# Optimization experiments

Measured on AMD Instinct MI355X. Metric: run time of the kernel, lower is better.

The kernel has to match this reference:

```python
import jax, jax.numpy as jnp
import numpy as np

MASK_ID = -100
L, D, HID, NH = 10, 768, 3072, 12
DH = D // NH
REACH = 2  # (sliding_window_size - 1) // 2 with window 5


def _layernorm(x, g, b, eps=1e-5):
    mu = x.mean(-1, keepdims=True)
    var = ((x - mu) ** 2).mean(-1, keepdims=True)
    return (x - mu) * jax.lax.rsqrt(var + eps) * g + b


def _adaln(x, temb, w, bb, g, be):
    # AdaLayerNormShiftScale: linear(silu(temb)) -> (scale, shift)
    e = jax.nn.silu(temb) @ w + bb
    scale, shift = jnp.split(e, 2, axis=-1)
    return _layernorm(x, g, be) * (1.0 + scale) + shift


def _timestep_emb(t):
    half = D // 2
    exponent = -np.log(10000.0) * jnp.arange(half, dtype=jnp.float32) / (half - 1.0)
    freq = jnp.exp(exponent)  # [half]
    emb = t.astype(jnp.float32)[..., None] * freq  # [b,s,half]
    return jnp.concatenate([jnp.sin(emb), jnp.cos(emb)], axis=-1)  # [b,s,D]


def setup_inputs():
    key = jax.random.key(0)
    ks = jax.random.split(key, 16)
    b, s = 4, 1024
    # packed token ids: 4 samples of 256 tokens (16x16 grid), last 64 tokens padding
    idx = np.arange(s)
    sid = idx // 256
    hpos = (idx % 256) // 16
    wpos = idx % 16
    sid = np.where(idx >= 960, MASK_ID, sid)
    tok = np.stack([sid, hpos, wpos], axis=-1)  # [s,3]
    token_ids = jnp.asarray(np.broadcast_to(tok, (b, s, 3)).copy(), dtype=jnp.int32)
    t = jax.random.randint(ks[0], (b, 1), 0, L + 1).astype(jnp.int32)
    t = jnp.broadcast_to(t, (b, s))

    def w(k, shape):
        return jax.random.normal(k, shape, jnp.float32) * 0.02

    return dict(
        x=jax.random.normal(ks[1], (b, s, D), jnp.float32),
        t=t,
        token_ids=token_ids,
        proj_in_w=w(ks[2], (D, D)), proj_in_b=jnp.zeros((D,), jnp.float32),
        h_emb=w(ks[3], (64, D)), w_emb=w(ks[4], (64, D)),
        adaln1_w=w(ks[5], (L, D, 2 * D)), adaln1_b=jnp.zeros((L, 2 * D), jnp.float32),
        ln1_g=jnp.ones((L, D), jnp.float32), ln1_b=jnp.zeros((L, D), jnp.float32),
        qkv_w=w(ks[6], (L, D, 3 * D)), qkv_b=jnp.zeros((L, 3 * D), jnp.float32),
        o_w=w(ks[7], (L, D, D)), o_b=jnp.zeros((L, D), jnp.float32),
        adaln2_w=w(ks[8], (L, D, 2 * D)), adaln2_b=jnp.zeros((L, 2 * D), jnp.float32),
        ln2_g=jnp.ones((L, D), jnp.float32), ln2_b=jnp.zeros((L, D), jnp.float32),
        fc1_w=w(ks[9], (L, D, HID)), fc1_b=jnp.zeros((L, HID), jnp.float32),
        fc2_w=w(ks[10], (L, HID, D)), fc2_b=jnp.zeros((L, D), jnp.float32),
        nout_w=w(ks[11], (D, 2 * D)), nout_b=jnp.zeros((2 * D,), jnp.float32),
        nout_g=jnp.ones((D,), jnp.float32), nout_beta=jnp.zeros((D,), jnp.float32),
    )


def _encoder(x, t, token_ids, proj_in_w, proj_in_b, h_emb, w_emb,
             adaln1_w, adaln1_b, ln1_g, ln1_b, qkv_w, qkv_b, o_w, o_b,
             adaln2_w, adaln2_b, ln2_g, ln2_b, fc1_w, fc1_b, fc2_w, fc2_b,
             nout_w, nout_b, nout_g, nout_beta):
    b, s, _ = x.shape
    sample_ids = token_ids[..., 0]          # [b,s]
    pos = token_ids[..., 1:]                # [b,s,2]
    x = x @ proj_in_w + proj_in_b
    x = x + h_emb[pos[..., 0]] + w_emb[pos[..., 1]]

    # block-sparse mask: same packed sample, Chebyshev sliding window, no padding queries
    same = sample_ids[:, :, None] == sample_ids[:, None, :]              # [b,s,s]
    cheby = jnp.abs(pos[:, :, None, :] - pos[:, None, :, :]).max(-1)      # [b,s,s]
    notpad_q = (sample_ids != MASK_ID)[:, :, None]
    mask = same & (cheby <= REACH) & notpad_q                             # [b,s,s]
    row_valid = mask.any(-1)[..., None]                                   # [b,s,1]

    temb = _timestep_emb(t)  # [b,s,D]
    scale = 1.0 / np.sqrt(DH)
    for i in range(L):
        h1 = _adaln(x, temb, adaln1_w[i], adaln1_b[i], ln1_g[i], ln1_b[i])
        qkv = h1 @ qkv_w[i] + qkv_b[i]
        q, k, v = jnp.split(qkv, 3, axis=-1)
        q = q.reshape(b, s, NH, DH)
        k = k.reshape(b, s, NH, DH)
        v = v.reshape(b, s, NH, DH)
        scores = jnp.einsum('bqhd,bkhd->bhqk', q, k) * scale
        scores = jnp.where(mask[:, None], scores, -1e30)
        attn = jax.nn.softmax(scores, axis=-1)
        o = jnp.einsum('bhqk,bkhd->bqhd', attn, v).reshape(b, s, D)
        o = jnp.where(row_valid, o, 0.0)  # fully-masked (padding) rows -> 0
        x = x + o @ o_w[i] + o_b[i]
        h2 = _adaln(x, temb, adaln2_w[i], adaln2_b[i], ln2_g[i], ln2_b[i])
        x = x + jax.nn.gelu(h2 @ fc1_w[i] + fc1_b[i], approximate=False) @ fc2_w[i] + fc2_b[i]
    x = _adaln(x, temb, nout_w, nout_b, nout_g, nout_beta)
    return x


def reference(x, t, token_ids, proj_in_w, proj_in_b, h_emb, w_emb,
              adaln1_w, adaln1_b, ln1_g, ln1_b, qkv_w, qkv_b, o_w, o_b,
              adaln2_w, adaln2_b, ln2_g, ln2_b, fc1_w, fc1_b, fc2_w, fc2_b,
              nout_w, nout_b, nout_g, nout_beta):
    return _encoder(x, t, token_ids, proj_in_w, proj_in_b, h_emb, w_emb,
                    adaln1_w, adaln1_b, ln1_g, ln1_b, qkv_w, qkv_b, o_w, o_b,
                    adaln2_w, adaln2_b, ln2_g, ln2_b, fc1_w, fc1_b, fc2_w, fc2_b,
                    nout_w, nout_b, nout_g, nout_beta)
```

## Files before the change

### kernel.cpp

```cpp
#include <hip/hip_runtime.h>
#include <hip/hip_bf16.h>
#include <math.h>

#define MASK_ID (-100)
#define SEQ 1024
#define BATCH 4
#define DMODEL 768
#define NHEAD 12
#define DHEAD 64
#define NLAYER 10
#define HIDDEN 3072

typedef unsigned short ushort_t;
typedef unsigned int uint_t;

__device__ __forceinline__ ushort_t f2bf(float f) {
    uint_t u = __float_as_uint(f);
    u = u + 0x7fffu + ((u >> 16) & 1u);
    return (ushort_t)(u >> 16);
}
__device__ __forceinline__ float bf2f(ushort_t u) {
    return __uint_as_float(((uint_t)u) << 16);
}

__device__ __forceinline__ void async_ld16(ushort_t* lds, const ushort_t* g) {
    __builtin_amdgcn_global_load_lds((__attribute__((address_space(1))) const void*)g,
                                     (__attribute__((address_space(3))) void*)lds, 16, 0, 0);
}

#define WAITVM(n) asm volatile("s_waitcnt vmcnt(" #n ")" ::: "memory")

__global__ void temb_silu_kernel(const int* __restrict__ t, float* __restrict__ stemb) {
    int b = blockIdx.x;
    int j = threadIdx.x;
    float tv = (float)t[b * SEQ];
    float freq = expf(-logf(10000.f) * (float)j / 383.f);
    float arg = tv * freq;
    float s = sinf(arg), c = cosf(arg);
    stemb[b * DMODEL + j]       = s / (1.f + expf(-s));
    stemb[b * DMODEL + 384 + j] = c / (1.f + expf(-c));
}

__global__ __launch_bounds__(256)
void adaln_partial_kernel(const float* __restrict__ stemb,
                          const float* __restrict__ a1w,
                          const float* __restrict__ a2w,
                          const float* __restrict__ nw,
                          float* __restrict__ partial) {
    int chunk = blockIdx.x;
    int kc    = blockIdx.y;
    int slot  = blockIdx.z;
    int tid = threadIdx.x;
    int col = chunk * 256 + tid;
    const float* W;
    if (slot == 20) W = nw;
    else {
        int i = slot >> 1;
        W = ((slot & 1) ? a2w : a1w) + (size_t)i * DMODEL * 2 * DMODEL;
    }
    __shared__ float sb[4 * 96];
    for (int idx = tid; idx < 4 * 96; idx += 256) {
        int bb = idx / 96, kk = idx % 96;
        sb[idx] = stemb[bb * DMODEL + kc * 96 + kk];
    }
    __syncthreads();
    const float* Wp = W + (size_t)(kc * 96) * (2 * DMODEL) + col;
    float a0 = 0.f, a1 = 0.f, a2 = 0.f, a3 = 0.f;
    #pragma unroll 4
    for (int kk = 0; kk < 96; ++kk) {
        float w = Wp[(size_t)kk * (2 * DMODEL)];
        a0 = fmaf(sb[kk], w, a0);
        a1 = fmaf(sb[96 + kk], w, a1);
        a2 = fmaf(sb[192 + kk], w, a2);
        a3 = fmaf(sb[288 + kk], w, a3);
    }
    size_t base = ((size_t)(slot * 8 + kc) * 4) * (2 * DMODEL) + col;
    partial[base + 0 * 2 * DMODEL] = a0;
    partial[base + 1 * 2 * DMODEL] = a1;
    partial[base + 2 * 2 * DMODEL] = a2;
    partial[base + 3 * 2 * DMODEL] = a3;
}

__global__ __launch_bounds__(256)
void adaln_reduce_kernel(const float* __restrict__ partial,
                         const float* __restrict__ a1b, const float* __restrict__ a2b,
                         const float* __restrict__ nb,
                         float* __restrict__ e_all) {
    int chunk = blockIdx.x;
    int slot  = blockIdx.y;
    int col = chunk * 256 + threadIdx.x;
    const float* bb;
    if (slot == 20) bb = nb;
    else {
        int i = slot >> 1;
        bb = ((slot & 1) ? a2b : a1b) + i * 2 * DMODEL;
    }
    float bias = bb[col];
    float s0 = bias, s1 = bias, s2 = bias, s3 = bias;
    #pragma unroll
    for (int kc = 0; kc < 8; ++kc) {
        size_t base = ((size_t)(slot * 8 + kc) * 4) * (2 * DMODEL) + col;
        s0 += partial[base + 0 * 2 * DMODEL];
        s1 += partial[base + 1 * 2 * DMODEL];
        s2 += partial[base + 2 * 2 * DMODEL];
        s3 += partial[base + 3 * 2 * DMODEL];
    }
    size_t o = (size_t)slot * 4 * (2 * DMODEL) + col;
    e_all[o + 0 * 2 * DMODEL] = s0;
    e_all[o + 1 * 2 * DMODEL] = s1;
    e_all[o + 2 * 2 * DMODEL] = s2;
    e_all[o + 3 * 2 * DMODEL] = s3;
}

__global__ __launch_bounds__(256)
void transpose_bf16_kernel(const float* __restrict__ in, ushort_t* __restrict__ out,
                           int R, int C) {
    __shared__ float tile[32][33];
    int tx = threadIdx.x & 31, ty = threadIdx.x >> 5;
    int c0 = blockIdx.x * 32, r0 = blockIdx.y * 32;
    #pragma unroll
    for (int i = 0; i < 4; ++i)
        tile[ty + 8 * i][tx] = in[(size_t)(r0 + ty + 8 * i) * C + c0 + tx];
    __syncthreads();
    #pragma unroll
    for (int i = 0; i < 4; ++i)
        out[(size_t)(c0 + ty + 8 * i) * R + r0 + tx] = f2bf(tile[tx][ty + 8 * i]);
}

__global__ __launch_bounds__(256)
void transpose_all_kernel(const float* __restrict__ w0, const float* __restrict__ w1,
                          const float* __restrict__ w2, const float* __restrict__ w3,
                          ushort_t* __restrict__ o0, ushort_t* __restrict__ o1,
                          ushort_t* __restrict__ o2, ushort_t* __restrict__ o3) {
    int layer = blockIdx.y;
    int id = blockIdx.x;
    const float* in; ushort_t* out; int R, C, tile_id, TX;
    if (id < 1728) {
        in = w0 + (size_t)layer * DMODEL * 3 * DMODEL; out = o0 + (size_t)layer * 3 * DMODEL * DMODEL;
        R = DMODEL; C = 3 * DMODEL; tile_id = id; TX = 72;
    } else if (id < 2304) {
        in = w1 + (size_t)layer * DMODEL * DMODEL; out = o1 + (size_t)layer * DMODEL * DMODEL;
        R = DMODEL; C = DMODEL; tile_id = id - 1728; TX = 24;
    } else if (id < 4608) {
        in = w2 + (size_t)layer * DMODEL * HIDDEN; out = o2 + (size_t)layer * HIDDEN * DMODEL;
        R = DMODEL; C = HIDDEN; tile_id = id - 2304; TX = 96;
    } else {
        in = w3 + (size_t)layer * HIDDEN * DMODEL; out = o3 + (size_t)layer * DMODEL * HIDDEN;
        R = HIDDEN; C = DMODEL; tile_id = id - 4608; TX = 24;
    }
    int c0 = (tile_id % TX) * 32, r0 = (tile_id / TX) * 32;
    __shared__ float tile[32][33];
    int tx = threadIdx.x & 31, ty = threadIdx.x >> 5;
    #pragma unroll
    for (int i = 0; i < 4; ++i)
        tile[ty + 8 * i][tx] = in[(size_t)(r0 + ty + 8 * i) * C + c0 + tx];
    __syncthreads();
    #pragma unroll
    for (int i = 0; i < 4; ++i)
        out[(size_t)(c0 + ty + 8 * i) * R + r0 + tx] = f2bf(tile[tx][ty + 8 * i]);
}

__global__ __launch_bounds__(256)
void f32_to_bf16_kernel(const float* __restrict__ in, ushort_t* __restrict__ out, int n8) {
    int i = blockIdx.x * 256 + threadIdx.x;
    if (i >= n8) return;
    float4 a = ((const float4*)in)[2 * i];
    float4 b = ((const float4*)in)[2 * i + 1];
    uint4 o;
    o.x = (uint_t)f2bf(a.x) | ((uint_t)f2bf(a.y) << 16);
    o.y = (uint_t)f2bf(a.z) | ((uint_t)f2bf(a.w) << 16);
    o.z = (uint_t)f2bf(b.x) | ((uint_t)f2bf(b.y) << 16);
    o.w = (uint_t)f2bf(b.z) | ((uint_t)f2bf(b.w) << 16);
    ((uint4*)out)[i] = o;
}

template<int OUT_BF>
__global__ __launch_bounds__(256)
void ln_adaln_kernel(const float* __restrict__ in, void* __restrict__ outv,
                     const float* __restrict__ g, const float* __restrict__ be,
                     const float* __restrict__ e) {
    int row = blockIdx.x;
    int b = row >> 10;
    const float* xr = in + (size_t)row * DMODEL;
    int tid = threadIdx.x;
    float v0 = xr[tid], v1 = xr[tid + 256], v2 = xr[tid + 512];
    float s = v0 + v1 + v2;
    float ss = v0 * v0 + v1 * v1 + v2 * v2;
    #pragma unroll
    for (int o = 32; o; o >>= 1) { s += __shfl_down(s, o); ss += __shfl_down(ss, o); }
    __shared__ float ls[4], lss[4];
    __shared__ float mu_s, rs_s;
    int wid = tid >> 6, lane = tid & 63;
    if (lane == 0) { ls[wid] = s; lss[wid] = ss; }
    __syncthreads();
    if (tid == 0) {
        float S = ls[0] + ls[1] + ls[2] + ls[3];
        float SS = lss[0] + lss[1] + lss[2] + lss[3];
        float mu = S * (1.f / DMODEL);
        float var = SS * (1.f / DMODEL) - mu * mu;
        mu_s = mu;
        rs_s = rsqrtf(var + 1e-5f);
    }
    __syncthreads();
    float mu = mu_s, rs = rs_s;
    const float* esc = e + (size_t)b * (2 * DMODEL);
    #pragma unroll
    for (int j = 0; j < 3; ++j) {
        int c = tid + j * 256;
        float v = (j == 0) ? v0 : (j == 1) ? v1 : v2;
        float y = (v - mu) * rs * g[c] + be[c];
        y = y * (1.f + esc[c]) + esc[DMODEL + c];
        if (OUT_BF) ((ushort_t*)outv)[(size_t)row * DMODEL + c] = f2bf(y);
        else        ((float*)outv)[(size_t)row * DMODEL + c] = y;
    }
}

__device__ __forceinline__ float gelu_exact(float x) {
    return 0.5f * x * (1.f + erff(x * 0.70710678118654752f));
}

template<int BM, int BN, int EPI>
__global__ __launch_bounds__(256, 2)
void gemm_bf16(const ushort_t* __restrict__ A, const ushort_t* __restrict__ Wt,
               const float* __restrict__ bias, void* __restrict__ outv,
               const float* __restrict__ emb_h, const float* __restrict__ emb_w,
               const int* __restrict__ tok,
               int M, int N, int K) {
    constexpr int WM = BM / 2, WN = BN / 2;
    constexpr int FM = WM / 16, FN = WN / 16;
    constexpr int BUF = (BM + BN) * 64;
    constexpr int LPT = (BM + BN) / 32;
    using f32x4  = __attribute__((ext_vector_type(4))) float;
    using bf16x8 = __attribute__((ext_vector_type(8))) short;

    __shared__ __align__(16) ushort_t lds[3 * BUF];

    int tid = threadIdx.x;
    int lane = tid & 63, wid = tid >> 6;
    int wr = wid >> 1, wc = wid & 1;
    int l16 = lane & 15, lg = lane >> 4;
    int sw = l16 & 7;

    int nx = N / BN;
    int cpx = gridDim.x >> 3;
    int wg = blockIdx.x;
    int wgid = (wg & 7) * cpx + (wg >> 3);
    int bx = wgid % nx, by = wgid / nx;
    int bm0 = by * BM, bn0 = bx * BN;

    f32x4 acc[FM][FN];
    #pragma unroll
    for (int m = 0; m < FM; ++m)
        #pragma unroll
        for (int n = 0; n < FN; ++n)
            #pragma unroll
            for (int r = 0; r < 4; ++r) acc[m][n][r] = 0.f;

    const ushort_t* Abase = A + (size_t)bm0 * K;
    const ushort_t* Bbase = Wt + (size_t)bn0 * K;

    #define STAGE(bufi, kt)                                                             \
        do {                                                                            \
            _Pragma("unroll")                                                           \
            for (int s2 = 0; s2 < BM / 32; ++s2) {                                      \
                int ca = s2 * 256 + tid;                                                \
                int rw = ca >> 3, kcs = (ca & 7) ^ (rw & 7);                            \
                async_ld16(&lds[(bufi) * BUF + ca * 8],                                 \
                           Abase + (size_t)rw * K + (kt) * 64 + kcs * 8);               \
            }                                                                           \
            _Pragma("unroll")                                                           \
            for (int s2 = 0; s2 < BN / 32; ++s2) {                                      \
                int ca = s2 * 256 + tid;                                                \
                int rw = ca >> 3, kcs = (ca & 7) ^ (rw & 7);                            \
                async_ld16(&lds[(bufi) * BUF + BM * 64 + ca * 8],                       \
                           Bbase + (size_t)rw * K + (kt) * 64 + kcs * 8);               \
            }                                                                           \
        } while (0)

    int nk = K >> 6;
    STAGE(0, 0);
    STAGE(1, 1);
    int bufi = 0;
    for (int kt = 0; kt < nk; ++kt) {
        int nxt = bufi + 2; if (nxt >= 3) nxt -= 3;
        if (kt + 2 < nk) {
            STAGE(nxt, kt + 2);
            if constexpr (LPT == 4) WAITVM(8); else WAITVM(12);
        } else if (kt + 1 < nk) {
            if constexpr (LPT == 4) WAITVM(4); else WAITVM(6);
        } else {
            WAITVM(0);
        }
        __builtin_amdgcn_s_barrier();
        __builtin_amdgcn_s_setprio(1);
        #pragma unroll
        for (int kk = 0; kk < 2; ++kk) {
            bf16x8 af[FM], bfr[FN];
            #pragma unroll
            for (int m = 0; m < FM; ++m) {
                int row = wr * WM + m * 16 + l16;
                int csw = (kk * 4 + lg) ^ sw;
                af[m] = *(const bf16x8*)&lds[bufi * BUF + row * 64 + csw * 8];
            }
            #pragma unroll
            for (int n = 0; n < FN; ++n) {
                int row = wc * WN + n * 16 + l16;
                int csw = (kk * 4 + lg) ^ sw;
                bfr[n] = *(const bf16x8*)&lds[bufi * BUF + BM * 64 + row * 64 + csw * 8];
            }
            #pragma unroll
            for (int m = 0; m < FM; ++m)
                #pragma unroll
                for (int n = 0; n < FN; ++n)
                    acc[m][n] = __builtin_amdgcn_mfma_f32_16x16x32_bf16(af[m], bfr[n], acc[m][n], 0, 0, 0);
        }
        __builtin_amdgcn_s_setprio(0);
        __builtin_amdgcn_s_barrier();
        ++bufi; if (bufi >= 3) bufi = 0;
    }
    #undef STAGE

    int r0 = bm0 + wr * WM, c0 = bn0 + wc * WN;
    #pragma unroll
    for (int m = 0; m < FM; ++m) {
        #pragma unroll
        for (int n = 0; n < FN; ++n) {
            int cc = c0 + n * 16 + l16;
            float bcol = bias[cc];
            #pragma unroll
            for (int r = 0; r < 4; ++r) {
                int row = r0 + m * 16 + lg * 4 + r;
                float v = acc[m][n][r] + bcol;
                if (EPI == 0) {
                    ((ushort_t*)outv)[(size_t)row * N + cc] = f2bf(v);
                } else if (EPI == 1) {
                    int p0 = tok[row * 3 + 1], p1 = tok[row * 3 + 2];
                    v += emb_h[p0 * DMODEL + cc] + emb_w[p1 * DMODEL + cc];
                    ((float*)outv)[(size_t)row * N + cc] = v;
                } else if (EPI == 2) {
                    float* op = (float*)outv + (size_t)row * N + cc;
                    *op = *op + v;
                } else {
                    ((ushort_t*)outv)[(size_t)row * N + cc] = f2bf(gelu_exact(v));
                }
            }
        }
    }
}

__global__ __launch_bounds__(256)
void attn_kernel(const ushort_t* __restrict__ qkv, const int* __restrict__ tok,
                 ushort_t* __restrict__ o_out) {
    int tid = threadIdx.x;
    int u = tid >> 2, part = tid & 3;
    int q = blockIdx.x * 16 + (u & 15);
    int h = blockIdx.y * 4 + (u >> 4);
    int b = blockIdx.z;
    int m = b * SEQ + q;
    ushort_t* op = o_out + (size_t)m * DMODEL + h * DHEAD + part * 16;
    int sid = tok[m * 3];
    if (sid == MASK_ID) {
        uint4 z = {0u, 0u, 0u, 0u};
        ((uint4*)op)[0] = z;
        ((uint4*)op)[1] = z;
        return;
    }
    int qh = tok[m * 3 + 1], qw = tok[m * 3 + 2];
    const ushort_t* qp = qkv + (size_t)m * (3 * DMODEL) + h * DHEAD + part * 16;
    float qv[16], ov[16];
    {
        uint4 u0 = ((const uint4*)qp)[0];
        uint4 u1 = ((const uint4*)qp)[1];
        qv[0] = bf2f(u0.x & 0xffff); qv[1] = bf2f(u0.x >> 16);
        qv[2] = bf2f(u0.y & 0xffff); qv[3] = bf2f(u0.y >> 16);
        qv[4] = bf2f(u0.z & 0xffff); qv[5] = bf2f(u0.z >> 16);
        qv[6] = bf2f(u0.w & 0xffff); qv[7] = bf2f(u0.w >> 16);
        qv[8]  = bf2f(u1.x & 0xffff); qv[9]  = bf2f(u1.x >> 16);
        qv[10] = bf2f(u1.y & 0xffff); qv[11] = bf2f(u1.y >> 16);
        qv[12] = bf2f(u1.z & 0xffff); qv[13] = bf2f(u1.z >> 16);
        qv[14] = bf2f(u1.w & 0xffff); qv[15] = bf2f(u1.w >> 16);
    }
    #pragma unroll
    for (int i = 0; i < 16; ++i) ov[i] = 0.f;
    float mx = -1e30f, den = 0.f;
    for (int dh = -2; dh <= 2; ++dh) {
        for (int dw = -2; dw <= 2; ++dw) {
            int kq = q + dh * 16 + dw;
            if (kq < 0 || kq >= SEQ) continue;
            int km = b * SEQ + kq;
            if (tok[km * 3] != sid) continue;
            int kh2 = tok[km * 3 + 1], kw2 = tok[km * 3 + 2];
            int adh = kh2 - qh; if (adh < 0) adh = -adh;
            int adw = kw2 - qw; if (adw < 0) adw = -adw;
            if (adh > 2 || adw > 2) continue;
            const ushort_t* kp = qkv + (size_t)km * (3 * DMODEL) + DMODEL + h * DHEAD + part * 16;
            float dot;
            {
                uint4 u0 = ((const uint4*)kp)[0];
                uint4 u1 = ((const uint4*)kp)[1];
                dot = qv[0] * bf2f(u0.x & 0xffff);
                dot = fmaf(qv[1], bf2f(u0.x >> 16), dot);
                dot = fmaf(qv[2], bf2f(u0.y & 0xffff), dot);
                dot = fmaf(qv[3], bf2f(u0.y >> 16), dot);
                dot = fmaf(qv[4], bf2f(u0.z & 0xffff), dot);
                dot = fmaf(qv[5], bf2f(u0.z >> 16), dot);
                dot = fmaf(qv[6], bf2f(u0.w & 0xffff), dot);
                dot = fmaf(qv[7], bf2f(u0.w >> 16), dot);
                dot = fmaf(qv[8],  bf2f(u1.x & 0xffff), dot);
                dot = fmaf(qv[9],  bf2f(u1.x >> 16), dot);
                dot = fmaf(qv[10], bf2f(u1.y & 0xffff), dot);
                dot = fmaf(qv[11], bf2f(u1.y >> 16), dot);
                dot = fmaf(qv[12], bf2f(u1.z & 0xffff), dot);
                dot = fmaf(qv[13], bf2f(u1.z >> 16), dot);
                dot = fmaf(qv[14], bf2f(u1.w & 0xffff), dot);
                dot = fmaf(qv[15], bf2f(u1.w >> 16), dot);
            }
            dot += __shfl_xor(dot, 1);
            dot += __shfl_xor(dot, 2);
            float sc = dot * 0.125f;
            float nm = fmaxf(mx, sc);
            float c1 = expf(mx - nm);
            float c2 = expf(sc - nm);
            den = den * c1 + c2;
            const ushort_t* vp = qkv + (size_t)km * (3 * DMODEL) + 2 * DMODEL + h * DHEAD + part * 16;
            {
                uint4 u0 = ((const uint4*)vp)[0];
                uint4 u1 = ((const uint4*)vp)[1];
                ov[0] = ov[0] * c1 + c2 * bf2f(u0.x & 0xffff);
                ov[1] = ov[1] * c1 + c2 * bf2f(u0.x >> 16);
                ov[2] = ov[2] * c1 + c2 * bf2f(u0.y & 0xffff);
                ov[3] = ov[3] * c1 + c2 * bf2f(u0.y >> 16);
                ov[4] = ov[4] * c1 + c2 * bf2f(u0.z & 0xffff);
                ov[5] = ov[5] * c1 + c2 * bf2f(u0.z >> 16);
                ov[6] = ov[6] * c1 + c2 * bf2f(u0.w & 0xffff);
                ov[7] = ov[7] * c1 + c2 * bf2f(u0.w >> 16);
                ov[8]  = ov[8]  * c1 + c2 * bf2f(u1.x & 0xffff);
                ov[9]  = ov[9]  * c1 + c2 * bf2f(u1.x >> 16);
                ov[10] = ov[10] * c1 + c2 * bf2f(u1.y & 0xffff);
                ov[11] = ov[11] * c1 + c2 * bf2f(u1.y >> 16);
                ov[12] = ov[12] * c1 + c2 * bf2f(u1.z & 0xffff);
                ov[13] = ov[13] * c1 + c2 * bf2f(u1.z >> 16);
                ov[14] = ov[14] * c1 + c2 * bf2f(u1.w & 0xffff);
                ov[15] = ov[15] * c1 + c2 * bf2f(u1.w >> 16);
            }
            mx = nm;
        }
    }
    float inv = 1.f / den;
    uint4 o0, o1;
    o0.x = (uint_t)f2bf(ov[0] * inv) | ((uint_t)f2bf(ov[1] * inv) << 16);
    o0.y = (uint_t)f2bf(ov[2] * inv) | ((uint_t)f2bf(ov[3] * inv) << 16);
    o0.z = (uint_t)f2bf(ov[4] * inv) | ((uint_t)f2bf(ov[5] * inv) << 16);
    o0.w = (uint_t)f2bf(ov[6] * inv) | ((uint_t)f2bf(ov[7] * inv) << 16);
    o1.x = (uint_t)f2bf(ov[8]  * inv) | ((uint_t)f2bf(ov[9]  * inv) << 16);
    o1.y = (uint_t)f2bf(ov[10] * inv) | ((uint_t)f2bf(ov[11] * inv) << 16);
    o1.z = (uint_t)f2bf(ov[12] * inv) | ((uint_t)f2bf(ov[13] * inv) << 16);
    o1.w = (uint_t)f2bf(ov[14] * inv) | ((uint_t)f2bf(ov[15] * inv) << 16);
    ((uint4*)op)[0] = o0;
    ((uint4*)op)[1] = o1;
}

extern "C" void kernel_launch(void* const* d_in, const int* in_sizes, int n_in,
                              void* d_out, int out_size, void* d_ws, size_t ws_size,
                              hipStream_t stream) {
    const float* x_in      = (const float*)d_in[0];
    const int*   t         = (const int*)d_in[1];
    const int*   tok       = (const int*)d_in[2];
    const float* proj_in_w = (const float*)d_in[3];
    const float* proj_in_b = (const float*)d_in[4];
    const float* h_emb     = (const float*)d_in[5];
    const float* w_emb     = (const float*)d_in[6];
    const float* adaln1_w  = (const float*)d_in[7];
    const float* adaln1_b  = (const float*)d_in[8];
    const float* ln1_g     = (const float*)d_in[9];
    const float* ln1_b     = (const float*)d_in[10];
    const float* qkv_w     = (const float*)d_in[11];
    const float* qkv_b     = (const float*)d_in[12];
    const float* o_w       = (const float*)d_in[13];
    const float* o_b       = (const float*)d_in[14];
    const float* adaln2_w  = (const float*)d_in[15];
    const float* adaln2_b  = (const float*)d_in[16];
    const float* ln2_g     = (const float*)d_in[17];
    const float* ln2_b     = (const float*)d_in[18];
    const float* fc1_w     = (const float*)d_in[19];
    const float* fc1_b     = (const float*)d_in[20];
    const float* fc2_w     = (const float*)d_in[21];
    const float* fc2_b     = (const float*)d_in[22];
    const float* nout_w    = (const float*)d_in[23];
    const float* nout_b    = (const float*)d_in[24];
    const float* nout_g    = (const float*)d_in[25];
    const float* nout_beta = (const float*)d_in[26];

    const int M = BATCH * SEQ;

    float* stemb   = (float*)d_ws;
    float* e_all   = stemb + BATCH * DMODEL;
    float* partial = e_all + 21 * BATCH * 2 * DMODEL;
    ushort_t* h_bf   = (ushort_t*)(partial + 21 * 8 * 4 * 2 * DMODEL);
    ushort_t* qkv_bf = h_bf + (size_t)M * DMODEL;
    ushort_t* hid_bf = qkv_bf + (size_t)M * 3 * DMODEL;
    ushort_t* projT  = hid_bf + (size_t)M * HIDDEN;
    ushort_t* qkvT_a = projT + (size_t)DMODEL * DMODEL;
    ushort_t* oT_a   = qkvT_a + (size_t)NLAYER * 3 * DMODEL * DMODEL;
    ushort_t* fc1T_a = oT_a + (size_t)NLAYER * DMODEL * DMODEL;
    ushort_t* fc2T_a = fc1T_a + (size_t)NLAYER * DMODEL * HIDDEN;
    float* x = (float*)d_out;

    temb_silu_kernel<<<BATCH, 384, 0, stream>>>(t, stemb);
    adaln_partial_kernel<<<dim3(6, 8, 2 * NLAYER + 1), 256, 0, stream>>>(
        stemb, adaln1_w, adaln2_w, nout_w, partial);
    adaln_reduce_kernel<<<dim3(6, 2 * NLAYER + 1), 256, 0, stream>>>(
        partial, adaln1_b, adaln2_b, nout_b, e_all);

    transpose_all_kernel<<<dim3(6912, NLAYER), 256, 0, stream>>>(
        qkv_w, o_w, fc1_w, fc2_w, qkvT_a, oT_a, fc1T_a, fc2T_a);
    transpose_bf16_kernel<<<dim3(DMODEL / 32, DMODEL / 32), 256, 0, stream>>>(proj_in_w, projT, DMODEL, DMODEL);

    f32_to_bf16_kernel<<<(M * DMODEL / 8 + 255) / 256, 256, 0, stream>>>(x_in, h_bf, M * DMODEL / 8);
    gemm_bf16<64, 64, 1><<<(DMODEL / 64) * (M / 64), 256, 0, stream>>>(
        h_bf, projT, proj_in_b, x, h_emb, w_emb, tok, M, DMODEL, DMODEL);

    for (int i = 0; i < NLAYER; ++i) {
        ln_adaln_kernel<1><<<M, 256, 0, stream>>>(
            x, h_bf, ln1_g + i * DMODEL, ln1_b + i * DMODEL,
            e_all + (size_t)(2 * i) * BATCH * 2 * DMODEL);
        gemm_bf16<64, 128, 0><<<(3 * DMODEL / 128) * (M / 64), 256, 0, stream>>>(
            h_bf, qkvT_a + (size_t)i * 3 * DMODEL * DMODEL, qkv_b + i * 3 * DMODEL,
            qkv_bf, nullptr, nullptr, nullptr, M, 3 * DMODEL, DMODEL);
        attn_kernel<<<dim3(SEQ / 16, NHEAD / 4, BATCH), 256, 0, stream>>>(qkv_bf, tok, h_bf);
        gemm_bf16<64, 64, 2><<<(DMODEL / 64) * (M / 64), 256, 0, stream>>>(
            h_bf, oT_a + (size_t)i * DMODEL * DMODEL, o_b + i * DMODEL,
            x, nullptr, nullptr, nullptr, M, DMODEL, DMODEL);
        ln_adaln_kernel<1><<<M, 256, 0, stream>>>(
            x, h_bf, ln2_g + i * DMODEL, ln2_b + i * DMODEL,
            e_all + (size_t)(2 * i + 1) * BATCH * 2 * DMODEL);
        gemm_bf16<64, 128, 3><<<(HIDDEN / 128) * (M / 64), 256, 0, stream>>>(
            h_bf, fc1T_a + (size_t)i * DMODEL * HIDDEN, fc1_b + i * HIDDEN,
            hid_bf, nullptr, nullptr, nullptr, M, HIDDEN, DMODEL);
        gemm_bf16<64, 64, 2><<<(DMODEL / 64) * (M / 64), 256, 0, stream>>>(
            hid_bf, fc2T_a + (size_t)i * DMODEL * HIDDEN, fc2_b + i * DMODEL,
            x, nullptr, nullptr, nullptr, M, DMODEL, HIDDEN);
    }

    ln_adaln_kernel<0><<<M, 256, 0, stream>>>(
        x, x, nout_g, nout_beta, e_all + (size_t)(2 * NLAYER) * BATCH * 2 * DMODEL);
}
```

Before: 1.847 ms.

## Enlarge transpose tiles, use wave-per-row layernorm, raise GEMM occupancy hint

The weight transpose kernel now moves 128x64 tiles per block and writes packed bf16 pairs, which cuts the block count and makes stores wider. The layernorm kernel now gives each wavefront one row and reduces with xor shuffles, with no shared memory or block barriers. The GEMM template gets an occupancy parameter, and the 64x64 GEMMs ask for 3 blocks per CU, which may limit registers and cause spills. The larger transpose tile uses about 33KB of LDS per block, which lowers that kernel's occupancy.

```diff
diff --git a/kernel.cpp b/kernel.cpp
--- a/kernel.cpp
+++ b/kernel.cpp
@@ -135,29 +135,37 @@
     int layer = blockIdx.y;
     int id = blockIdx.x;
     const float* in; ushort_t* out; int R, C, tile_id, TX;
-    if (id < 1728) {
+    if (id < 216) {
         in = w0 + (size_t)layer * DMODEL * 3 * DMODEL; out = o0 + (size_t)layer * 3 * DMODEL * DMODEL;
-        R = DMODEL; C = 3 * DMODEL; tile_id = id; TX = 72;
-    } else if (id < 2304) {
+        R = DMODEL; C = 3 * DMODEL; tile_id = id; TX = 36;
+    } else if (id < 288) {
         in = w1 + (size_t)layer * DMODEL * DMODEL; out = o1 + (size_t)layer * DMODEL * DMODEL;
-        R = DMODEL; C = DMODEL; tile_id = id - 1728; TX = 24;
-    } else if (id < 4608) {
+        R = DMODEL; C = DMODEL; tile_id = id - 216; TX = 12;
+    } else if (id < 576) {
         in = w2 + (size_t)layer * DMODEL * HIDDEN; out = o2 + (size_t)layer * HIDDEN * DMODEL;
-        R = DMODEL; C = HIDDEN; tile_id = id - 2304; TX = 96;
+        R = DMODEL; C = HIDDEN; tile_id = id - 288; TX = 48;
     } else {
         in = w3 + (size_t)layer * HIDDEN * DMODEL; out = o3 + (size_t)layer * DMODEL * HIDDEN;
-        R = HIDDEN; C = DMODEL; tile_id = id - 4608; TX = 24;
-    }
-    int c0 = (tile_id % TX) * 32, r0 = (tile_id / TX) * 32;
-    __shared__ float tile[32][33];
-    int tx = threadIdx.x & 31, ty = threadIdx.x >> 5;
-    #pragma unroll
-    for (int i = 0; i < 4; ++i)
-        tile[ty + 8 * i][tx] = in[(size_t)(r0 + ty + 8 * i) * C + c0 + tx];
+        R = HIDDEN; C = DMODEL; tile_id = id - 576; TX = 12;
+    }
+    int c0 = (tile_id % TX) * 64, r0 = (tile_id / TX) * 128;
+    __shared__ float tl[128][65];
+    int tid = threadIdx.x;
+    #pragma unroll
+    for (int i = 0; i < 32; ++i) {
+        int idx = i * 256 + tid;
+        int r = idx >> 6, c = idx & 63;
+        tl[r][c] = in[(size_t)(r0 + r) * C + c0 + c];
+    }
     __syncthreads();
     #pragma unroll
-    for (int i = 0; i < 4; ++i)
-        out[(size_t)(c0 + ty + 8 * i) * R + r0 + tx] = f2bf(tile[tx][ty + 8 * i]);
+    for (int j = 0; j < 16; ++j) {
+        int idx = j * 256 + tid;
+        int oc = idx >> 6, pr = idx & 63;
+        float a = tl[pr * 2][oc], b = tl[pr * 2 + 1][oc];
+        uint_t pk = (uint_t)f2bf(a) | ((uint_t)f2bf(b) << 16);
+        *(uint_t*)&out[(size_t)(c0 + oc) * R + r0 + pr * 2] = pk;
+    }
 }
 
 __global__ __launch_bounds__(256)
@@ -179,36 +187,28 @@
 void ln_adaln_kernel(const float* __restrict__ in, void* __restrict__ outv,
                      const float* __restrict__ g, const float* __restrict__ be,
                      const float* __restrict__ e) {
-    int row = blockIdx.x;
+    int wid = threadIdx.x >> 6, lane = threadIdx.x & 63;
+    int row = blockIdx.x * 4 + wid;
     int b = row >> 10;
     const float* xr = in + (size_t)row * DMODEL;
-    int tid = threadIdx.x;
-    float v0 = xr[tid], v1 = xr[tid + 256], v2 = xr[tid + 512];
-    float s = v0 + v1 + v2;
-    float ss = v0 * v0 + v1 * v1 + v2 * v2;
-    #pragma unroll
-    for (int o = 32; o; o >>= 1) { s += __shfl_down(s, o); ss += __shfl_down(ss, o); }
-    __shared__ float ls[4], lss[4];
-    __shared__ float mu_s, rs_s;
-    int wid = tid >> 6, lane = tid & 63;
-    if (lane == 0) { ls[wid] = s; lss[wid] = ss; }
-    __syncthreads();
-    if (tid == 0) {
-        float S = ls[0] + ls[1] + ls[2] + ls[3];
-        float SS = lss[0] + lss[1] + lss[2] + lss[3];
-        float mu = S * (1.f / DMODEL);
-        float var = SS * (1.f / DMODEL) - mu * mu;
-        mu_s = mu;
-        rs_s = rsqrtf(var + 1e-5f);
-    }
-    __syncthreads();
-    float mu = mu_s, rs = rs_s;
+    float v[12];
+    float s = 0.f, ss = 0.f;
+    #pragma unroll
+    for (int j = 0; j < 12; ++j) {
+        v[j] = xr[lane + j * 64];
+        s += v[j];
+        ss = fmaf(v[j], v[j], ss);
+    }
+    #pragma unroll
+    for (int o = 1; o < 64; o <<= 1) { s += __shfl_xor(s, o); ss += __shfl_xor(ss, o); }
+    float mu = s * (1.f / DMODEL);
+    float var = ss * (1.f / DMODEL) - mu * mu;
+    float rs = rsqrtf(var + 1e-5f);
     const float* esc = e + (size_t)b * (2 * DMODEL);
     #pragma unroll
-    for (int j = 0; j < 3; ++j) {
-        int c = tid + j * 256;
-        float v = (j == 0) ? v0 : (j == 1) ? v1 : v2;
-        float y = (v - mu) * rs * g[c] + be[c];
+    for (int j = 0; j < 12; ++j) {
+        int c = lane + j * 64;
+        float y = (v[j] - mu) * rs * g[c] + be[c];
         y = y * (1.f + esc[c]) + esc[DMODEL + c];
         if (OUT_BF) ((ushort_t*)outv)[(size_t)row * DMODEL + c] = f2bf(y);
         else        ((float*)outv)[(size_t)row * DMODEL + c] = y;
@@ -219,8 +219,8 @@
     return 0.5f * x * (1.f + erff(x * 0.70710678118654752f));
 }
 
-template<int BM, int BN, int EPI>
-__global__ __launch_bounds__(256, 2)
+template<int BM, int BN, int EPI, int OCC>
+__global__ __launch_bounds__(256, OCC)
 void gemm_bf16(const ushort_t* __restrict__ A, const ushort_t* __restrict__ Wt,
                const float* __restrict__ bias, void* __restrict__ outv,
                const float* __restrict__ emb_h, const float* __restrict__ emb_w,
@@ -512,36 +512,36 @@
     adaln_reduce_kernel<<<dim3(6, 2 * NLAYER + 1), 256, 0, stream>>>(
         partial, adaln1_b, adaln2_b, nout_b, e_all);
 
-    transpose_all_kernel<<<dim3(6912, NLAYER), 256, 0, stream>>>(
+    transpose_all_kernel<<<dim3(864, NLAYER), 256, 0, stream>>>(
         qkv_w, o_w, fc1_w, fc2_w, qkvT_a, oT_a, fc1T_a, fc2T_a);
     transpose_bf16_kernel<<<dim3(DMODEL / 32, DMODEL / 32), 256, 0, stream>>>(proj_in_w, projT, DMODEL, DMODEL);
 
     f32_to_bf16_kernel<<<(M * DMODEL / 8 + 255) / 256, 256, 0, stream>>>(x_in, h_bf, M * DMODEL / 8);
-    gemm_bf16<64, 64, 1><<<(DMODEL / 64) * (M / 64), 256, 0, stream>>>(
+    gemm_bf16<64, 64, 1, 3><<<(DMODEL / 64) * (M / 64), 256, 0, stream>>>(
         h_bf, projT, proj_in_b, x, h_emb, w_emb, tok, M, DMODEL, DMODEL);
 
     for (int i = 0; i < NLAYER; ++i) {
-        ln_adaln_kernel<1><<<M, 256, 0, stream>>>(
+        ln_adaln_kernel<1><<<M / 4, 256, 0, stream>>>(
             x, h_bf, ln1_g + i * DMODEL, ln1_b + i * DMODEL,
             e_all + (size_t)(2 * i) * BATCH * 2 * DMODEL);
-        gemm_bf16<64, 128, 0><<<(3 * DMODEL / 128) * (M / 64), 256, 0, stream>>>(
+        gemm_bf16<64, 128, 0, 2><<<(3 * DMODEL / 128) * (M / 64), 256, 0, stream>>>(
             h_bf, qkvT_a + (size_t)i * 3 * DMODEL * DMODEL, qkv_b + i * 3 * DMODEL,
             qkv_bf, nullptr, nullptr, nullptr, M, 3 * DMODEL, DMODEL);
         attn_kernel<<<dim3(SEQ / 16, NHEAD / 4, BATCH), 256, 0, stream>>>(qkv_bf, tok, h_bf);
-        gemm_bf16<64, 64, 2><<<(DMODEL / 64) * (M / 64), 256, 0, stream>>>(
+        gemm_bf16<64, 64, 2, 3><<<(DMODEL / 64) * (M / 64), 256, 0, stream>>>(
             h_bf, oT_a + (size_t)i * DMODEL * DMODEL, o_b + i * DMODEL,
             x, nullptr, nullptr, nullptr, M, DMODEL, DMODEL);
-        ln_adaln_kernel<1><<<M, 256, 0, stream>>>(
+        ln_adaln_kernel<1><<<M / 4, 256, 0, stream>>>(
             x, h_bf, ln2_g + i * DMODEL, ln2_b + i * DMODEL,
             e_all + (size_t)(2 * i + 1) * BATCH * 2 * DMODEL);
-        gemm_bf16<64, 128, 3><<<(HIDDEN / 128) * (M / 64), 256, 0, stream>>>(
+        gemm_bf16<64, 128, 3, 2><<<(HIDDEN / 128) * (M / 64), 256, 0, stream>>>(
             h_bf, fc1T_a + (size_t)i * DMODEL * HIDDEN, fc1_b + i * HIDDEN,
             hid_bf, nullptr, nullptr, nullptr, M, HIDDEN, DMODEL);
-        gemm_bf16<64, 64, 2><<<(DMODEL / 64) * (M / 64), 256, 0, stream>>>(
+        gemm_bf16<64, 64, 2, 3><<<(DMODEL / 64) * (M / 64), 256, 0, stream>>>(
             hid_bf, fc2T_a + (size_t)i * DMODEL * HIDDEN, fc2_b + i * DMODEL,
             x, nullptr, nullptr, nullptr, M, DMODEL, HIDDEN);
     }
 
-    ln_adaln_kernel<0><<<M, 256, 0, stream>>>(
+    ln_adaln_kernel<0><<<M / 4, 256, 0, stream>>>(
         x, x, nout_g, nout_beta, e_all + (size_t)(2 * NLAYER) * BATCH * 2 * DMODEL);
 }
```

Result: no change. 1.839 ms (-0.4%).
